# Optimization experiments

Measured on AMD Instinct MI355X. Metric: run time of the kernel, lower is better.

The kernel has to match this reference:

```python
import jax, jax.numpy as jnp
import numpy as np

D = 1024      # hidden_size
F = 4096      # intermediate_size
E = 16        # num_experts
TOPK = 2      # num_experts_per_tok
B, L = 1, 2048


def setup_inputs() -> dict:
    key = jax.random.key(0)
    ks = jax.random.split(key, 5)
    s = 0.02
    return {
        "x": jax.random.normal(ks[0], (B, L, D), dtype=jnp.float32),
        "gate_w": jax.random.normal(ks[1], (E, D), dtype=jnp.float32) * s,
        "w1s": jax.random.normal(ks[2], (E, F, D), dtype=jnp.float32) * s,  # per-expert w1 (out,in)
        "w2s": jax.random.normal(ks[3], (E, D, F), dtype=jnp.float32) * s,  # per-expert w2
        "w3s": jax.random.normal(ks[4], (E, F, D), dtype=jnp.float32) * s,  # per-expert w3
    }


def reference(x, gate_w, w1s, w2s, w3s):
    b, l, d = x.shape
    xf = x.reshape(-1, d)                                   # [T, D]
    router_logits = xf @ gate_w.T                           # [T, E]
    topw, topi = jax.lax.top_k(router_logits.astype(jnp.float32), TOPK)
    topw = jax.nn.softmax(topw, axis=-1).astype(x.dtype)    # [T, K]
    T = xf.shape[0]
    # dense combine weights: zero for unselected experts (same math as masked loop)
    combine = jnp.zeros((T, E), x.dtype).at[jnp.arange(T)[:, None], topi].add(topw)

    def body(acc, ew):
        w1, w2, w3, cw = ew                                 # cw: [T]
        h = jax.nn.silu(xf @ w1.T) * (xf @ w3.T)            # [T, F]
        return acc + cw[:, None] * (h @ w2.T), None

    out, _ = jax.lax.scan(body, jnp.zeros_like(xf), (w1s, w2s, w3s, combine.T))
    return out.reshape(b, l, d), router_logits
```

## Files before the change

kernel.cpp:

```cpp
#include <hip/hip_runtime.h>

#define D_DIM 1024
#define F_DIM 4096
#define E_NUM 16
#define T_NUM 2048

typedef __bf16 bf16x8 __attribute__((ext_vector_type(8)));
typedef float f32x4 __attribute__((ext_vector_type(4)));

__device__ __forceinline__ unsigned pack2bf(float a, float b) {
  unsigned ua = __builtin_bit_cast(unsigned, a);
  unsigned ub = __builtin_bit_cast(unsigned, b);
  return ((ub + 0x8000u) & 0xffff0000u) | ((ua + 0x8000u) >> 16);
}
__device__ __forceinline__ unsigned short f2bf(float a) {
  unsigned ua = __builtin_bit_cast(unsigned, a);
  return (unsigned short)((ua + 0x8000u) >> 16);
}
__device__ __forceinline__ bf16x8 cvt8(f32x4 a, f32x4 b) {
  union { unsigned u[4]; bf16x8 v; } r;
  r.u[0] = pack2bf(a[0], a[1]); r.u[1] = pack2bf(a[2], a[3]);
  r.u[2] = pack2bf(b[0], b[1]); r.u[3] = pack2bf(b[2], b[3]);
  return r.v;
}
__device__ __forceinline__ void gload16(const void* g, void* l) {
  __builtin_amdgcn_global_load_lds(
      (const __attribute__((address_space(1))) unsigned*)g,
      (__attribute__((address_space(3))) unsigned*)l, 16, 0, 0);
}

__global__ __launch_bounds__(256) void moe_xcast(
    const float* __restrict__ x, unsigned short* __restrict__ xbf)
{
  int i = blockIdx.x * 256 + threadIdx.x;
  const f32x4* p = (const f32x4*)x + (size_t)i * 2;
  f32x4 a = p[0], b = p[1];
  uint4 o;
  o.x = pack2bf(a[0], a[1]); o.y = pack2bf(a[2], a[3]);
  o.z = pack2bf(b[0], b[1]); o.w = pack2bf(b[2], b[3]);
  ((uint4*)xbf)[i] = o;
}

__global__ __launch_bounds__(256) void moe_router(
    const float* __restrict__ x, const float* __restrict__ gate,
    float* __restrict__ logits_out, int* __restrict__ topi, float* __restrict__ topw)
{
  __shared__ float lg[16][17];
  int tid = threadIdx.x;
  int tbase = blockIdx.x * 16;
  int tt = tid >> 4, e = tid & 15;
  const float4* xr = (const float4*)(x + (size_t)(tbase + tt) * D_DIM);
  const float4* gw = (const float4*)(gate + (size_t)e * D_DIM);
  float acc = 0.f;
  #pragma unroll 4
  for (int k = 0; k < D_DIM / 4; ++k) {
    float4 a = xr[k], b = gw[k];
    acc += a.x * b.x + a.y * b.y + a.z * b.z + a.w * b.w;
  }
  lg[tt][e] = acc;
  logits_out[(size_t)(tbase + tt) * E_NUM + e] = acc;
  __syncthreads();
  if (tid < 16) {
    int t = tid;
    float best = -1e30f; int i0 = 0;
    #pragma unroll
    for (int j = 0; j < 16; ++j) { float v = lg[t][j]; if (v > best) { best = v; i0 = j; } }
    float best1 = -1e30f; int i1 = 0;
    #pragma unroll
    for (int j = 0; j < 16; ++j) { if (j == i0) continue; float v = lg[t][j]; if (v > best1) { best1 = v; i1 = j; } }
    float e1 = __expf(best1 - best);
    float inv = 1.f / (1.f + e1);
    int gt = tbase + t;
    topi[gt * 2]     = i0;  topi[gt * 2 + 1] = i1;
    topw[gt * 2]     = inv; topw[gt * 2 + 1] = e1 * inv;
  }
}

__global__ __launch_bounds__(1024) void moe_route_build(
    const int* __restrict__ topi,
    int* __restrict__ cnt, int* __restrict__ rowbase,
    int* __restrict__ rowlist, int* __restrict__ rowpos)
{
  __shared__ int scnt[16];
  __shared__ int sbase[17];
  int wave = threadIdx.x >> 6;
  int lane = threadIdx.x & 63;
  int total = 0;
  for (int c = 0; c < (T_NUM * 2) / 64; ++c) {
    int s = c * 64 + lane;
    unsigned long long m = __ballot(topi[s] == wave);
    total += __popcll(m);
  }
  if (lane == 0) scnt[wave] = total;
  __syncthreads();
  if (threadIdx.x == 0) {
    int acc = 0;
    for (int e2 = 0; e2 < 16; ++e2) { sbase[e2] = acc; cnt[e2] = scnt[e2]; acc += scnt[e2]; }
    sbase[16] = acc;
    for (int e2 = 0; e2 <= 16; ++e2) rowbase[e2] = sbase[e2];
  }
  __syncthreads();
  int running = sbase[wave];
  for (int c = 0; c < (T_NUM * 2) / 64; ++c) {
    int s = c * 64 + lane;
    int ei = topi[s];
    unsigned long long m = __ballot(ei == wave);
    if (ei == wave) {
      int pos = running + __popcll(m & ((1ull << lane) - 1ull));
      rowlist[pos] = s;
      rowpos[s] = pos;
    }
    running += __popcll(m);
  }
}

__global__ __launch_bounds__(256, 2) void moe_gemm1(
    const unsigned short* __restrict__ xbf, const float* __restrict__ w1s, const float* __restrict__ w3s,
    const int* __restrict__ cnt, const int* __restrict__ rowbase, const int* __restrict__ rowlist,
    unsigned short* __restrict__ H)
{
  int e = blockIdx.z, mt = blockIdx.y, nt = blockIdx.x;
  int Ne = cnt[e];
  if (mt * 128 >= Ne) return;
  int rbase = rowbase[e];

  __shared__ char smem[81920];

  int tid = threadIdx.x, lane = tid & 63, wave = tid >> 6;

  const char* px[2];
  #pragma unroll
  for (int it = 0; it < 2; ++it) {
    int r = (wave * 2 + it) * 16 + (lane >> 2);
    int lr = mt * 128 + r;
    int tok = (lr < Ne) ? (rowlist[rbase + lr] >> 1) : 0;
    int c = (lane & 3) ^ (r & 3);
    px[it] = (const char*)(xbf + (size_t)tok * D_DIM) + c * 16;
  }
  const float* w1e = w1s + (size_t)e * F_DIM * D_DIM + (size_t)(nt * 128) * D_DIM;
  const float* w3e = w3s + (size_t)e * F_DIM * D_DIM + (size_t)(nt * 128) * D_DIM;
  const char* p1[4]; const char* p3[4];
  #pragma unroll
  for (int it = 0; it < 4; ++it) {
    int r = (wave * 4 + it) * 8 + (lane >> 3);
    int c = (lane & 7) ^ (r & 7);
    p1[it] = (const char*)(w1e + (size_t)r * D_DIM) + c * 16;
    p3[it] = (const char*)(w3e + (size_t)r * D_DIM) + c * 16;
  }

  int wm = wave >> 1, wn = wave & 1;
  int lr16 = lane & 15, lq = lane >> 4;

  unsigned offA[4];
  #pragma unroll
  for (int mi = 0; mi < 4; ++mi) {
    int m = wm * 64 + mi * 16 + lr16;
    offA[mi] = (unsigned)(m * 64 + ((lq ^ (m & 3)) * 16));
  }
  unsigned offB[4][2];
  #pragma unroll
  for (int ni = 0; ni < 4; ++ni) {
    int n = wn * 64 + ni * 16 + lr16;
    #pragma unroll
    for (int h = 0; h < 2; ++h)
      offB[ni][h] = (unsigned)(n * 128 + (((lq * 2 + h) ^ (n & 7)) * 16));
  }

  f32x4 acc1[4][4], acc3[4][4];
  #pragma unroll
  for (int i = 0; i < 4; ++i)
    #pragma unroll
    for (int j = 0; j < 4; ++j) { acc1[i][j] = {0.f,0.f,0.f,0.f}; acc3[i][j] = {0.f,0.f,0.f,0.f}; }

  unsigned xdst = (unsigned)((wave * 2) * 1024 + lane * 16);
  unsigned wdst = (unsigned)((wave * 4) * 1024 + lane * 16);

  auto STAGE = [&](unsigned bsel, int ks) {
    gload16(px[0] + ks * 64, smem + bsel * 8192 + xdst);
    gload16(px[1] + ks * 64, smem + bsel * 8192 + xdst + 1024);
    #pragma unroll
    for (int it = 0; it < 4; ++it) {
      gload16(p1[it] + ks * 128, smem + 16384 + bsel * 16384 + wdst + it * 1024);
      gload16(p3[it] + ks * 128, smem + 49152 + bsel * 16384 + wdst + it * 1024);
    }
  };

  STAGE(0, 0);
  __syncthreads();
  unsigned buf = 0;
  for (int ks = 0; ks < 32; ++ks) {
    if (ks < 31) STAGE(buf ^ 1u, ks + 1);
    unsigned xb = buf * 8192;
    unsigned w1b = 16384 + buf * 16384;
    unsigned w3b = 49152 + buf * 16384;
    bf16x8 af[4], b1f[4], b3f[4];
    #pragma unroll
    for (int mi = 0; mi < 4; ++mi)
      af[mi] = *(const bf16x8*)(smem + xb + offA[mi]);
    #pragma unroll
    for (int ni = 0; ni < 4; ++ni) {
      b1f[ni] = cvt8(*(const f32x4*)(smem + w1b + offB[ni][0]),
                     *(const f32x4*)(smem + w1b + offB[ni][1]));
      b3f[ni] = cvt8(*(const f32x4*)(smem + w3b + offB[ni][0]),
                     *(const f32x4*)(smem + w3b + offB[ni][1]));
    }
    #pragma unroll
    for (int ni = 0; ni < 4; ++ni)
      #pragma unroll
      for (int mi = 0; mi < 4; ++mi) {
        acc1[mi][ni] = __builtin_amdgcn_mfma_f32_16x16x32_bf16(af[mi], b1f[ni], acc1[mi][ni], 0, 0, 0);
        acc3[mi][ni] = __builtin_amdgcn_mfma_f32_16x16x32_bf16(af[mi], b3f[ni], acc3[mi][ni], 0, 0, 0);
      }
    __syncthreads();
    buf ^= 1u;
  }

  #pragma unroll
  for (int mi = 0; mi < 4; ++mi) {
    int mb = wm * 64 + mi * 16 + lq * 4;
    #pragma unroll
    for (int r = 0; r < 4; ++r) {
      int lrow = mt * 128 + mb + r;
      if (lrow < Ne) {
        size_t hrow = (size_t)(rbase + lrow) * F_DIM;
        #pragma unroll
        for (int ni = 0; ni < 4; ++ni) {
          int f = nt * 128 + wn * 64 + ni * 16 + lr16;
          float a1v = acc1[mi][ni][r];
          float a3v = acc3[mi][ni][r];
          float hv = (a1v / (1.f + __expf(-a1v))) * a3v;
          H[hrow + f] = f2bf(hv);
        }
      }
    }
  }
}

__global__ __launch_bounds__(256, 2) void moe_gemm2(
    const unsigned short* __restrict__ H, const float* __restrict__ w2s,
    const int* __restrict__ cnt, const int* __restrict__ rowbase,
    unsigned short* __restrict__ Ybf)
{
  int e = blockIdx.z, mt = blockIdx.y, nt = blockIdx.x;
  int Ne = cnt[e];
  if (mt * 128 >= Ne) return;
  int rbase = rowbase[e];

  __shared__ char smem[65536];

  int tid = threadIdx.x, lane = tid & 63, wave = tid >> 6;

  const char* pa[4];
  #pragma unroll
  for (int it = 0; it < 4; ++it) {
    int r = (wave * 4 + it) * 8 + (lane >> 3);
    int c = (lane & 7) ^ (r & 7);
    int grow = mt * 128 + r; if (grow >= Ne) grow = Ne - 1;
    pa[it] = (const char*)(H + (size_t)(rbase + grow) * F_DIM) + c * 16;
  }
  const float* w2e = w2s + (size_t)e * D_DIM * F_DIM + (size_t)(nt * 64) * F_DIM;
  const char* pb[4];
  #pragma unroll
  for (int it = 0; it < 4; ++it) {
    int r = (wave * 4 + it) * 4 + (lane >> 4);
    int c = (lane & 15) ^ (r & 7);
    pb[it] = (const char*)(w2e + (size_t)r * F_DIM) + c * 16;
  }

  int wm = wave >> 1, wn = wave & 1;
  int lr16 = lane & 15, lq = lane >> 4;

  f32x4 acc[4][2];
  #pragma unroll
  for (int i = 0; i < 4; ++i) { acc[i][0] = {0.f,0.f,0.f,0.f}; acc[i][1] = {0.f,0.f,0.f,0.f}; }

  unsigned dst = (unsigned)((wave * 4) * 1024 + lane * 16);

  auto STAGE = [&](unsigned bsel, int ks) {
    #pragma unroll
    for (int it = 0; it < 4; ++it) {
      gload16(pa[it] + ks * 128, smem + bsel * 16384 + dst + it * 1024);
      gload16(pb[it] + ks * 256, smem + 32768 + bsel * 16384 + dst + it * 1024);
    }
  };

  STAGE(0, 0);
  __syncthreads();
  unsigned buf = 0;
  for (int ks = 0; ks < 64; ++ks) {
    if (ks < 63) STAGE(buf ^ 1u, ks + 1);
    unsigned ab = buf * 16384;
    unsigned bb = 32768 + buf * 16384;
    #pragma unroll
    for (int ksub = 0; ksub < 2; ++ksub) {
      bf16x8 af[4], bf[2];
      #pragma unroll
      for (int mi = 0; mi < 4; ++mi) {
        int m = wm * 64 + mi * 16 + lr16;
        unsigned off = (unsigned)(m * 128 + (((ksub * 4 + lq) ^ (m & 7)) * 16));
        af[mi] = *(const bf16x8*)(smem + ab + off);
      }
      #pragma unroll
      for (int ni = 0; ni < 2; ++ni) {
        int n = wn * 32 + ni * 16 + lr16;
        unsigned o0 = (unsigned)(n * 256 + (((ksub * 8 + lq * 2 + 0) ^ (n & 7)) * 16));
        unsigned o1 = (unsigned)(n * 256 + (((ksub * 8 + lq * 2 + 1) ^ (n & 7)) * 16));
        bf[ni] = cvt8(*(const f32x4*)(smem + bb + o0), *(const f32x4*)(smem + bb + o1));
      }
      #pragma unroll
      for (int mi = 0; mi < 4; ++mi)
        #pragma unroll
        for (int ni = 0; ni < 2; ++ni)
          acc[mi][ni] = __builtin_amdgcn_mfma_f32_16x16x32_bf16(af[mi], bf[ni], acc[mi][ni], 0, 0, 0);
    }
    __syncthreads();
    buf ^= 1u;
  }

  #pragma unroll
  for (int mi = 0; mi < 4; ++mi) {
    int mb = wm * 64 + mi * 16 + lq * 4;
    #pragma unroll
    for (int r = 0; r < 4; ++r) {
      int lrow = mt * 128 + mb + r;
      if (lrow < Ne) {
        size_t yrow = (size_t)(rbase + lrow) * D_DIM;
        #pragma unroll
        for (int ni = 0; ni < 2; ++ni) {
          int d = nt * 64 + wn * 32 + ni * 16 + lr16;
          Ybf[yrow + d] = f2bf(acc[mi][ni][r]);
        }
      }
    }
  }
}

__global__ __launch_bounds__(128) void moe_combine(
    const unsigned short* __restrict__ Ybf, const int* __restrict__ rowpos,
    const float* __restrict__ topw, float* __restrict__ out)
{
  int t = blockIdx.x, tid = threadIdx.x;
  int r0 = rowpos[t * 2], r1 = rowpos[t * 2 + 1];
  float p0 = topw[t * 2], p1 = topw[t * 2 + 1];
  uint4 a = ((const uint4*)(Ybf + (size_t)r0 * D_DIM))[tid];
  uint4 b = ((const uint4*)(Ybf + (size_t)r1 * D_DIM))[tid];
  float4 o0, o1;
  #define LO(u) __builtin_bit_cast(float, (unsigned)((u) << 16))
  #define HI(u) __builtin_bit_cast(float, (unsigned)((u) & 0xffff0000u))
  o0.x = p0 * LO(a.x) + p1 * LO(b.x);  o0.y = p0 * HI(a.x) + p1 * HI(b.x);
  o0.z = p0 * LO(a.y) + p1 * LO(b.y);  o0.w = p0 * HI(a.y) + p1 * HI(b.y);
  o1.x = p0 * LO(a.z) + p1 * LO(b.z);  o1.y = p0 * HI(a.z) + p1 * HI(b.z);
  o1.z = p0 * LO(a.w) + p1 * LO(b.w);  o1.w = p0 * HI(a.w) + p1 * HI(b.w);
  #undef LO
  #undef HI
  float4* orow = (float4*)(out + (size_t)t * D_DIM);
  orow[tid * 2]     = o0;
  orow[tid * 2 + 1] = o1;
}

extern "C" void kernel_launch(void* const* d_in, const int* in_sizes, int n_in,
                              void* d_out, int out_size, void* d_ws, size_t ws_size,
                              hipStream_t stream) {
  const float* x    = (const float*)d_in[0];
  const float* gate = (const float*)d_in[1];
  const float* w1   = (const float*)d_in[2];
  const float* w2   = (const float*)d_in[3];
  const float* w3   = (const float*)d_in[4];
  float* out    = (float*)d_out;
  float* logits = out + (size_t)T_NUM * D_DIM;

  char* ws = (char*)d_ws;
  int*   cnt     = (int*)(ws + 0);
  int*   rowbase = (int*)(ws + 64);
  int*   topi    = (int*)(ws + 1024);
  float* topw    = (float*)(ws + 1024 + 16384);
  int*   rowlist = (int*)(ws + 1024 + 32768);
  int*   rowpos  = (int*)(ws + 1024 + 49152);
  unsigned short* H   = (unsigned short*)(ws + 131072);
  unsigned short* Ybf = (unsigned short*)(ws + 131072 + 33554432);
  unsigned short* xbf = (unsigned short*)(ws + 131072 + 33554432 + 8388608);

  moe_xcast<<<(T_NUM * D_DIM) / (256 * 8), 256, 0, stream>>>(x, xbf);
  moe_router<<<T_NUM / 16, 256, 0, stream>>>(x, gate, logits, topi, topw);
  moe_route_build<<<1, 1024, 0, stream>>>(topi, cnt, rowbase, rowlist, rowpos);
  moe_gemm1<<<dim3(F_DIM / 128, T_NUM / 128, E_NUM), 256, 0, stream>>>(xbf, w1, w3, cnt, rowbase, rowlist, H);
  moe_gemm2<<<dim3(D_DIM / 64, T_NUM / 128, E_NUM), 256, 0, stream>>>(H, w2, cnt, rowbase, Ybf);
  moe_combine<<<T_NUM, 128, 0, stream>>>(Ybf, rowpos, topw, out);
}
```

Measured before the change: 367.9 us.

## Overlap next-stage global loads with compute using partial vmcnt waits

Replaces the __syncthreads after staging with explicit s_waitcnt vmcnt(N) followed by raw s_barrier in both GEMM kernels. The intent is to wait only for the current buffer's async loads while the next stage's loads remain in flight, instead of draining all outstanding loads each iteration. It also changes the fp32-to-bf16 conversion to native casts, which may map to hardware convert instructions, and changes the LDS XOR swizzle of the x tile to use (row>>1) to reduce bank conflicts. Raw barriers without a full waitcnt risk ordering bugs if the compiler emits the loads in a different count or order than assumed.

New measurement: 365.7 us. No clear change (-0.6%).

```diff
diff --git a/kernel.cpp b/kernel.cpp
--- a/kernel.cpp
+++ b/kernel.cpp
@@ -18,10 +18,10 @@
   return (unsigned short)((ua + 0x8000u) >> 16);
 }
 __device__ __forceinline__ bf16x8 cvt8(f32x4 a, f32x4 b) {
-  union { unsigned u[4]; bf16x8 v; } r;
-  r.u[0] = pack2bf(a[0], a[1]); r.u[1] = pack2bf(a[2], a[3]);
-  r.u[2] = pack2bf(b[0], b[1]); r.u[3] = pack2bf(b[2], b[3]);
-  return r.v;
+  bf16x8 r;
+  r[0] = (__bf16)a[0]; r[1] = (__bf16)a[1]; r[2] = (__bf16)a[2]; r[3] = (__bf16)a[3];
+  r[4] = (__bf16)b[0]; r[5] = (__bf16)b[1]; r[6] = (__bf16)b[2]; r[7] = (__bf16)b[3];
+  return r;
 }
 __device__ __forceinline__ void gload16(const void* g, void* l) {
   __builtin_amdgcn_global_load_lds(
@@ -134,7 +134,7 @@
     int r = (wave * 2 + it) * 16 + (lane >> 2);
     int lr = mt * 128 + r;
     int tok = (lr < Ne) ? (rowlist[rbase + lr] >> 1) : 0;
-    int c = (lane & 3) ^ (r & 3);
+    int c = (lane & 3) ^ ((r >> 1) & 3);
     px[it] = (const char*)(xbf + (size_t)tok * D_DIM) + c * 16;
   }
   const float* w1e = w1s + (size_t)e * F_DIM * D_DIM + (size_t)(nt * 128) * D_DIM;
@@ -155,7 +155,7 @@
   #pragma unroll
   for (int mi = 0; mi < 4; ++mi) {
     int m = wm * 64 + mi * 16 + lr16;
-    offA[mi] = (unsigned)(m * 64 + ((lq ^ (m & 3)) * 16));
+    offA[mi] = (unsigned)(m * 64 + ((lq ^ ((m >> 1) & 3)) * 16));
   }
   unsigned offB[4][2];
   #pragma unroll
@@ -186,10 +186,15 @@
   };
 
   STAGE(0, 0);
-  __syncthreads();
   unsigned buf = 0;
   for (int ks = 0; ks < 32; ++ks) {
-    if (ks < 31) STAGE(buf ^ 1u, ks + 1);
+    if (ks < 31) {
+      STAGE(buf ^ 1u, ks + 1);
+      asm volatile("s_waitcnt vmcnt(10)" ::: "memory");
+    } else {
+      asm volatile("s_waitcnt vmcnt(0)" ::: "memory");
+    }
+    __builtin_amdgcn_s_barrier();
     unsigned xb = buf * 8192;
     unsigned w1b = 16384 + buf * 16384;
     unsigned w3b = 49152 + buf * 16384;
@@ -211,7 +216,7 @@
         acc1[mi][ni] = __builtin_amdgcn_mfma_f32_16x16x32_bf16(af[mi], b1f[ni], acc1[mi][ni], 0, 0, 0);
         acc3[mi][ni] = __builtin_amdgcn_mfma_f32_16x16x32_bf16(af[mi], b3f[ni], acc3[mi][ni], 0, 0, 0);
       }
-    __syncthreads();
+    __builtin_amdgcn_s_barrier();
     buf ^= 1u;
   }
 
@@ -285,10 +290,15 @@
   };
 
   STAGE(0, 0);
-  __syncthreads();
   unsigned buf = 0;
   for (int ks = 0; ks < 64; ++ks) {
-    if (ks < 63) STAGE(buf ^ 1u, ks + 1);
+    if (ks < 63) {
+      STAGE(buf ^ 1u, ks + 1);
+      asm volatile("s_waitcnt vmcnt(8)" ::: "memory");
+    } else {
+      asm volatile("s_waitcnt vmcnt(0)" ::: "memory");
+    }
+    __builtin_amdgcn_s_barrier();
     unsigned ab = buf * 16384;
     unsigned bb = 32768 + buf * 16384;
     #pragma unroll
@@ -313,7 +323,7 @@
         for (int ni = 0; ni < 2; ++ni)
           acc[mi][ni] = __builtin_amdgcn_mfma_f32_16x16x32_bf16(af[mi], bf[ni], acc[mi][ni], 0, 0, 0);
     }
-    __syncthreads();
+    __builtin_amdgcn_s_barrier();
     buf ^= 1u;
   }
 
```
